# Kernel optimization log

Measured on AMD Instinct MI355X. Metric: run time of the kernel, lower is better.

## Reference

```python
import jax, jax.numpy as jnp
import numpy as np

EMB_DIM = 4096
N_HEADS = 32
QKV_DIM = EMB_DIM // N_HEADS  # 128
B, S = 4, 4096


def setup_inputs() -> dict:
    key = jax.random.key(0)
    ks = jax.random.split(key, 7)
    std = 1.0 / np.sqrt(EMB_DIM)  # lecun-normal-ish init for DenseGeneral kernels
    x = jax.random.normal(ks[0], (B, S, EMB_DIM), dtype=jnp.float32)
    Wq = jax.random.normal(ks[1], (EMB_DIM, QKV_DIM, N_HEADS), dtype=jnp.float32) * std
    bq = jnp.zeros((QKV_DIM, N_HEADS), dtype=jnp.float32)
    Wk = jax.random.normal(ks[2], (EMB_DIM, QKV_DIM, 1), dtype=jnp.float32) * std
    bk = jnp.zeros((QKV_DIM, 1), dtype=jnp.float32)
    Wv = jax.random.normal(ks[3], (EMB_DIM, QKV_DIM, 1), dtype=jnp.float32) * std
    bv = jnp.zeros((QKV_DIM, 1), dtype=jnp.float32)
    return {"x": x, "Wq": Wq, "bq": bq, "Wk": Wk, "bk": bk, "Wv": Wv, "bv": bv}


def reference(x, Wq, bq, Wk, bk, Wv, bv):
    # q: (B, S, d, h) ; k, v: (B, S, d) -- single shared head (squeeze the 1-axis)
    q = jnp.einsum('bsD,Ddh->bsdh', x, Wq) + bq
    k = (jnp.einsum('bsD,Ddh->bsdh', x, Wk) + bk)[..., 0]
    v = (jnp.einsum('bsD,Ddh->bsdh', x, Wv) + bv)[..., 0]
    qkv_dim = q.shape[-2]
    n_heads = q.shape[-1]
    scale = 1.0 / jnp.sqrt(jnp.asarray(qkv_dim, dtype=q.dtype))
    # Original: scores = q @ swapaxes(repeat(k), -1, -2) -> contracts the HEADS
    # axis per token. With k repeated across heads this equals
    # (sum_h q[..., d, h]) * k[..., e]. einsum sums h (absent from output).
    scores = jnp.einsum('bsdh,bse->bsde', q, k) * scale  # (B, S, d, d)
    p = jax.nn.softmax(scores, axis=-1)
    # out[..., d, h] = sum_e p[..., d, e] * v_rep[..., e, h]; v identical per h.
    o = jnp.einsum('bsde,bse->bsd', p, v)  # (B, S, d)
    out = jnp.broadcast_to(o[..., None], o.shape + (n_heads,))  # (B, S, d, h)
    return out.reshape(x.shape[:-1] + (qkv_dim * n_heads,))
```

## Files before the change

### kernel.cpp

```cpp
#include <hip/hip_runtime.h>

#define EMB  4096
#define DH   128
#define NH   32
#define NTOK 16384
#define NCOL 384

#define BM 64
#define BK 64

typedef __attribute__((ext_vector_type(8))) short short8;
typedef __attribute__((ext_vector_type(4))) short short4_t;
typedef __attribute__((ext_vector_type(4))) float f32x4;

static __device__ __forceinline__ unsigned int cvt2(float a, float b) {
    unsigned int r;
    asm volatile("v_cvt_pk_bf16_f32 %0, %1, %2" : "=v"(r) : "v"(a), "v"(b));
    return r;
}
static __device__ __forceinline__ unsigned short f2bf(float f) {
    unsigned int u = __builtin_bit_cast(unsigned int, f);
    u += 0x7fffu + ((u >> 16) & 1u);
    return (unsigned short)(u >> 16);
}
static __device__ __forceinline__ float exp2_hw(float x) {
#if __has_builtin(__builtin_amdgcn_exp2f)
    return __builtin_amdgcn_exp2f(x);
#else
    float r;
    asm volatile("v_exp_f32 %0, %1\n\ts_nop 1" : "=v"(r) : "v"(x));
    return r;
#endif
}

__global__ void prep_w(const float* __restrict__ Wq, const float* __restrict__ bq,
                       const float* __restrict__ Wk, const float* __restrict__ bk,
                       const float* __restrict__ Wv, const float* __restrict__ bv,
                       unsigned short* __restrict__ W3F, float* __restrict__ bias) {
    const int tid = blockIdx.x * 256 + threadIdx.x;
    const int n  = tid >> 9;
    const int ck = tid & 511;
    const int D0 = ck * 8;

    float v[8];
    if (n < DH) {
#pragma unroll
        for (int e = 0; e < 8; ++e) {
            const float4* p = (const float4*)(Wq + (size_t)(D0 + e) * (DH * NH) + n * NH);
            float s = 0.f;
#pragma unroll
            for (int i = 0; i < 8; ++i) { float4 q = p[i]; s += (q.x + q.y) + (q.z + q.w); }
            v[e] = s;
        }
    } else if (n < 2 * DH) {
#pragma unroll
        for (int e = 0; e < 8; ++e) v[e] = Wk[(size_t)(D0 + e) * DH + (n - DH)];
    } else {
#pragma unroll
        for (int e = 0; e < 8; ++e) v[e] = Wv[(size_t)(D0 + e) * DH + (n - 2 * DH)];
    }

    union { short8 s; unsigned int u[4]; } pk;
#pragma unroll
    for (int j = 0; j < 4; ++j)
        pk.u[j] = (unsigned int)f2bf(v[2 * j]) | ((unsigned int)f2bf(v[2 * j + 1]) << 16);

    const int p    = n >> 6, r = n & 63;
    const int jfr  = r >> 4, lmod = r & 15;
    const int kt   = ck >> 3;
    const int kh   = (ck >> 2) & 1;
    const int lgrp = ck & 3;
    const int lane = lgrp * 16 + lmod;
    char* dst = (char*)W3F + (size_t)p * 524288 + (size_t)kt * 8192
              + (kh * 4 + jfr) * 1024 + lane * 16;
    *(short8*)dst = pk.s;

    if (ck == 0) {
        float b;
        if (n < DH) {
            float s = 0.f;
#pragma unroll
            for (int h = 0; h < NH; ++h) s += bq[n * NH + h];
            b = s;
        } else if (n < 2 * DH) {
            b = bk[n - DH];
        } else {
            b = bv[n - 2 * DH];
        }
        bias[n] = b;
    }
}

__global__ __launch_bounds__(384) void fused_mqa(const float* __restrict__ X,
                         const unsigned short* __restrict__ W3F,
                         const float* __restrict__ bias,
                         float* __restrict__ out) {
    __shared__ __align__(16) unsigned short Asm[BM * BK];
    __shared__ float qsm[32 * NCOL];

    const int bid  = blockIdx.x;
    const int wkid = (bid & 7) * 32 + (bid >> 3);
    const int m0   = wkid * BM;
    const int nt   = EMB / BK;

    const int t = threadIdx.x, lane = t & 63, w = t >> 6;
    const int lmod = lane & 15, lgrp = lane >> 4;

    f32x4 acc[4][4] = {};

    const int arow4 = lane >> 4;
    const float* xp = X + (size_t)(m0 + w * 16 + arow4) * EMB + (lane & 15) * 4;
    const int acs = (lane & 15) >> 1;
    const int ah4 = (lane & 1) * 4;

    const char* bsrc = (const char*)W3F + (size_t)w * 524288 + lane * 16;

    f32x4 avA[4], avB[4];
    short8 bfA[8], bfB[8];

#define LOAD_AV(T, AV) do { \
    const int tc_ = (T) < nt ? (T) : nt - 1; \
    _Pragma("unroll") \
    for (int i = 0; i < 4; ++i) \
        AV[i] = __builtin_nontemporal_load((const f32x4*)(xp + tc_ * BK + i * 4 * EMB)); \
} while (0)

#define LOAD_BF(T, BF) do { \
    const int tc_ = (T) < nt ? (T) : nt - 1; \
    const char* bt_ = bsrc + (size_t)tc_ * 8192; \
    _Pragma("unroll") \
    for (int j = 0; j < 8; ++j) \
        BF[j] = *(const short8*)(bt_ + j * 1024); \
} while (0)

#define WRITE_A(AV) do { \
    _Pragma("unroll") \
    for (int idx = 0; idx < 4; ++idx) { \
        const int rl = w * 16 + idx * 4 + arow4; \
        union { short4_t s; unsigned int u[2]; } pk; \
        pk.u[0] = cvt2(AV[idx].x, AV[idx].y); \
        pk.u[1] = cvt2(AV[idx].z, AV[idx].w); \
        *(short4_t*)(&Asm[rl * BK + ((acs ^ (rl & 7)) << 3) + ah4]) = pk.s; \
    } \
} while (0)

#define COMPUTE(BF) do { \
    _Pragma("unroll") \
    for (int kh = 0; kh < 2; ++kh) { \
        const int cs = ((kh * 4 + lgrp) ^ (lmod & 7)) * 8; \
        short8 af[4]; \
        _Pragma("unroll") \
        for (int i = 0; i < 4; ++i) \
            af[i] = *(const short8*)(&Asm[(i * 16 + lmod) * BK + cs]); \
        _Pragma("unroll") \
        for (int i = 0; i < 4; ++i) \
            _Pragma("unroll") \
            for (int j = 0; j < 4; ++j) \
                acc[i][j] = __builtin_amdgcn_mfma_f32_16x16x32_bf16(af[i], BF[kh * 4 + j], acc[i][j], 0, 0, 0); \
    } \
} while (0)

#define ABAR()  do { __builtin_amdgcn_s_barrier(); } while (0)
#define WBAR()  do { asm volatile("s_waitcnt lgkmcnt(0)" ::: "memory"); \
                     __builtin_amdgcn_s_barrier(); } while (0)

    if (w < 4) { LOAD_AV(0, avA); LOAD_AV(1, avB); }
    LOAD_BF(0, bfA);

    for (int tt = 0; tt < nt; tt += 2) {
        ABAR();
        if (w < 4) WRITE_A(avA);
        WBAR();
        LOAD_BF(tt + 1, bfB);
        if (w < 4) LOAD_AV(tt + 2, avA);
        COMPUTE(bfA);
        ABAR();
        if (w < 4) WRITE_A(avB);
        WBAR();
        LOAD_BF(tt + 2, bfA);
        if (w < 4) LOAD_AV(tt + 3, avB);
        COMPUTE(bfB);
    }

    const float c = 0.088388347648318447f * 1.4426950408889634f;
#pragma unroll
    for (int pass = 0; pass < 2; ++pass) {
        __syncthreads();
#pragma unroll
        for (int j = 0; j < 4; ++j) {
            const int col = w * 64 + j * 16 + lmod;
            const float bj = bias[col];
#pragma unroll
            for (int i2 = 0; i2 < 2; ++i2) {
                const int row = i2 * 16 + (lgrp << 2);
#pragma unroll
                for (int r = 0; r < 4; ++r)
                    qsm[(row + r) * NCOL + col] = acc[pass * 2 + i2][j][r] + bj;
            }
        }
        __syncthreads();

        for (int tok = w; tok < 32; tok += 6) {
            const float* row = &qsm[tok * NCOL];
            const float q0  = row[lane],       q1  = row[64 + lane];
            const float kk0 = row[128 + lane], kk1 = row[192 + lane];

            float lmax = fmaxf(kk0, kk1), lmin = fminf(kk0, kk1);
#pragma unroll
            for (int off = 32; off; off >>= 1) {
                lmax = fmaxf(lmax, __shfl_xor(lmax, off));
                lmin = fminf(lmin, __shfl_xor(lmin, off));
            }

            const float a0 = q0 * c, a1 = q1 * c;
            const float m0v = (a0 >= 0.f) ? a0 * lmax : a0 * lmin;
            const float m1v = (a1 >= 0.f) ? a1 * lmax : a1 * lmin;

            float s00 = 0.f, s01 = 0.f, s10 = 0.f, s11 = 0.f;
#pragma unroll 8
            for (int e = 0; e < DH; ++e) {
                const float kv = row[128 + e];
                const float vv = row[256 + e];
                const float p0 = exp2_hw(fmaf(a0, kv, -m0v));
                const float p1 = exp2_hw(fmaf(a1, kv, -m1v));
                s00 += p0;  s01 = fmaf(p0, vv, s01);
                s10 += p1;  s11 = fmaf(p1, vv, s11);
            }
            const float o0 = s01 / s00;
            const float o1 = s11 / s10;

            float* orow = out + (size_t)(m0 + pass * 32 + tok) * (DH * NH);
#pragma unroll
            for (int it = 0; it < 16; ++it) {
                const int idx = it * 64 + lane;
                const int src = (it & 7) * 8 + (lane >> 3);
                const float val = (it < 8) ? __shfl(o0, src) : __shfl(o1, src);
                f32x4 f4 = {val, val, val, val};
                __builtin_nontemporal_store(f4, (f32x4*)(orow + idx * 4));
            }
        }
    }
#undef LOAD_AV
#undef LOAD_BF
#undef WRITE_A
#undef COMPUTE
#undef ABAR
#undef WBAR
}

extern "C" void kernel_launch(void* const* d_in, const int* in_sizes, int n_in,
                              void* d_out, int out_size, void* d_ws, size_t ws_size,
                              hipStream_t stream) {
    const float* x  = (const float*)d_in[0];
    const float* Wq = (const float*)d_in[1];
    const float* bq = (const float*)d_in[2];
    const float* Wk = (const float*)d_in[3];
    const float* bk = (const float*)d_in[4];
    const float* Wv = (const float*)d_in[5];
    const float* bv = (const float*)d_in[6];
    float* out = (float*)d_out;

    char* ws = (char*)d_ws;
    unsigned short* W3F = (unsigned short*)ws;
    float* bias = (float*)(ws + 3145728);

    prep_w<<<(NCOL * 512) / 256, 256, 0, stream>>>(Wq, bq, Wk, bk, Wv, bv, W3F, bias);
    fused_mqa<<<NTOK / BM, 384, 0, stream>>>(x, W3F, bias, out);
}
```

Measured before the change: 163.6 us.

## Split fused MQA work across 8 waves with 48 output columns each

Raises the block from 6 to 8 wavefronts. Each wave now owns 48 of the 384 output columns instead of 64, and all waves share the A-tile global load and bf16 conversion instead of only four doing it. The B-fragment addressing is remapped so that each wave fetches three 16-column fragments per k-half, and the epilogue token loop strides by 8. The aim is more latency hiding and fewer registers per wave, at the cost of more waves per barrier and smaller per-wave MFMA tiles with less operand reuse.

```diff
diff --git a/kernel.cpp b/kernel.cpp
--- a/kernel.cpp
+++ b/kernel.cpp
@@ -91,7 +91,7 @@
     }
 }
 
-__global__ __launch_bounds__(384) void fused_mqa(const float* __restrict__ X,
+__global__ __launch_bounds__(512) void fused_mqa(const float* __restrict__ X,
                          const unsigned short* __restrict__ W3F,
                          const float* __restrict__ bias,
                          float* __restrict__ out) {
@@ -106,42 +106,44 @@
     const int t = threadIdx.x, lane = t & 63, w = t >> 6;
     const int lmod = lane & 15, lgrp = lane >> 4;
 
-    f32x4 acc[4][4] = {};
-
-    const int arow4 = lane >> 4;
-    const float* xp = X + (size_t)(m0 + w * 16 + arow4) * EMB + (lane & 15) * 4;
-    const int acs = (lane & 15) >> 1;
-    const int ah4 = (lane & 1) * 4;
-
-    const char* bsrc = (const char*)W3F + (size_t)w * 524288 + lane * 16;
-
-    f32x4 avA[4], avB[4];
-    short8 bfA[8], bfB[8];
+    f32x4 acc[4][3] = {};
+
+    const int arow = w * 8 + (lane >> 3);
+    const float* xp = X + (size_t)(m0 + arow) * EMB + (lane & 7) * 4;
+    const int ac0 = (lane & 7) >> 1;
+    const int ah4 = ((lane & 7) & 1) * 4;
+
+    const char* bp[3];
+#pragma unroll
+    for (int j = 0; j < 3; ++j) {
+        const int f = w * 3 + j;
+        bp[j] = (const char*)W3F + (size_t)(f >> 2) * 524288 + (f & 3) * 1024 + lane * 16;
+    }
+
+    f32x4 avA[2], avB[2];
+    short8 bfA[6], bfB[6];
 
 #define LOAD_AV(T, AV) do { \
     const int tc_ = (T) < nt ? (T) : nt - 1; \
-    _Pragma("unroll") \
-    for (int i = 0; i < 4; ++i) \
-        AV[i] = __builtin_nontemporal_load((const f32x4*)(xp + tc_ * BK + i * 4 * EMB)); \
+    AV[0] = __builtin_nontemporal_load((const f32x4*)(xp + tc_ * BK)); \
+    AV[1] = __builtin_nontemporal_load((const f32x4*)(xp + tc_ * BK + 32)); \
 } while (0)
 
 #define LOAD_BF(T, BF) do { \
     const int tc_ = (T) < nt ? (T) : nt - 1; \
-    const char* bt_ = bsrc + (size_t)tc_ * 8192; \
     _Pragma("unroll") \
-    for (int j = 0; j < 8; ++j) \
-        BF[j] = *(const short8*)(bt_ + j * 1024); \
+    for (int j = 0; j < 3; ++j) { \
+        BF[j]     = *(const short8*)(bp[j] + (size_t)tc_ * 8192); \
+        BF[3 + j] = *(const short8*)(bp[j] + (size_t)tc_ * 8192 + 4096); \
+    } \
 } while (0)
 
 #define WRITE_A(AV) do { \
-    _Pragma("unroll") \
-    for (int idx = 0; idx < 4; ++idx) { \
-        const int rl = w * 16 + idx * 4 + arow4; \
-        union { short4_t s; unsigned int u[2]; } pk; \
-        pk.u[0] = cvt2(AV[idx].x, AV[idx].y); \
-        pk.u[1] = cvt2(AV[idx].z, AV[idx].w); \
-        *(short4_t*)(&Asm[rl * BK + ((acs ^ (rl & 7)) << 3) + ah4]) = pk.s; \
-    } \
+    union { short4_t s; unsigned int u[2]; } p0, p1; \
+    p0.u[0] = cvt2(AV[0].x, AV[0].y);  p0.u[1] = cvt2(AV[0].z, AV[0].w); \
+    p1.u[0] = cvt2(AV[1].x, AV[1].y);  p1.u[1] = cvt2(AV[1].z, AV[1].w); \
+    *(short4_t*)(&Asm[arow * BK + ((ac0 ^ (arow & 7)) << 3) + ah4]) = p0.s; \
+    *(short4_t*)(&Asm[arow * BK + (((ac0 + 4) ^ (arow & 7)) << 3) + ah4]) = p1.s; \
 } while (0)
 
 #define COMPUTE(BF) do { \
@@ -155,30 +157,30 @@
         _Pragma("unroll") \
         for (int i = 0; i < 4; ++i) \
             _Pragma("unroll") \
-            for (int j = 0; j < 4; ++j) \
-                acc[i][j] = __builtin_amdgcn_mfma_f32_16x16x32_bf16(af[i], BF[kh * 4 + j], acc[i][j], 0, 0, 0); \
+            for (int j = 0; j < 3; ++j) \
+                acc[i][j] = __builtin_amdgcn_mfma_f32_16x16x32_bf16(af[i], BF[kh * 3 + j], acc[i][j], 0, 0, 0); \
     } \
 } while (0)
 
-#define ABAR()  do { __builtin_amdgcn_s_barrier(); } while (0)
-#define WBAR()  do { asm volatile("s_waitcnt lgkmcnt(0)" ::: "memory"); \
-                     __builtin_amdgcn_s_barrier(); } while (0)
-
-    if (w < 4) { LOAD_AV(0, avA); LOAD_AV(1, avB); }
+#define ABAR()  do { asm volatile("s_barrier" ::: "memory"); } while (0)
+#define WBAR()  do { asm volatile("s_waitcnt lgkmcnt(0)\n\ts_barrier" ::: "memory"); } while (0)
+
+    LOAD_AV(0, avA);
+    LOAD_AV(1, avB);
     LOAD_BF(0, bfA);
 
     for (int tt = 0; tt < nt; tt += 2) {
         ABAR();
-        if (w < 4) WRITE_A(avA);
+        WRITE_A(avA);
         WBAR();
         LOAD_BF(tt + 1, bfB);
-        if (w < 4) LOAD_AV(tt + 2, avA);
+        LOAD_AV(tt + 2, avA);
         COMPUTE(bfA);
         ABAR();
-        if (w < 4) WRITE_A(avB);
+        WRITE_A(avB);
         WBAR();
         LOAD_BF(tt + 2, bfA);
-        if (w < 4) LOAD_AV(tt + 3, avB);
+        LOAD_AV(tt + 3, avB);
         COMPUTE(bfB);
     }
 
@@ -187,8 +189,8 @@
     for (int pass = 0; pass < 2; ++pass) {
         __syncthreads();
 #pragma unroll
-        for (int j = 0; j < 4; ++j) {
-            const int col = w * 64 + j * 16 + lmod;
+        for (int j = 0; j < 3; ++j) {
+            const int col = w * 48 + j * 16 + lmod;
             const float bj = bias[col];
 #pragma unroll
             for (int i2 = 0; i2 < 2; ++i2) {
@@ -200,7 +202,7 @@
         }
         __syncthreads();
 
-        for (int tok = w; tok < 32; tok += 6) {
+        for (int tok = w; tok < 32; tok += 8) {
             const float* row = &qsm[tok * NCOL];
             const float q0  = row[lane],       q1  = row[64 + lane];
             const float kk0 = row[128 + lane], kk1 = row[192 + lane];
@@ -265,5 +267,5 @@
     float* bias = (float*)(ws + 3145728);
 
     prep_w<<<(NCOL * 512) / 256, 256, 0, stream>>>(Wq, bq, Wk, bk, Wv, bv, W3F, bias);
-    fused_mqa<<<NTOK / BM, 384, 0, stream>>>(x, W3F, bias, out);
-}
+    fused_mqa<<<NTOK / BM, 512, 0, stream>>>(x, W3F, bias, out);
+}
```

Result: no change. 160.5 us (-1.9%).
